# Optimization experiments

Measured on AMD Instinct MI355X. Metric: run time of the kernel, lower is better.

The kernel has to match this reference:

```python
import jax, jax.numpy as jnp
import numpy as np

S, B, D, H = 2048, 16, 1024, 1024


def setup_inputs() -> dict:
    key = jax.random.key(0)
    k1, k2, k3 = jax.random.split(key, 3)
    X = jax.random.normal(k1, (S, B, D), dtype=jnp.float32)
    hidden = jax.random.normal(k2, (B, H), dtype=jnp.float32)
    W = jax.random.normal(k3, (3 * H, D), dtype=jnp.float32) * 0.02  # nn.Linear weight [out,in]
    b = jnp.zeros((3 * H,), dtype=jnp.float32)
    return {"X": X, "hidden": hidden, "W": W, "b": b}


def reference(X, hidden, W, b):
    # window=1: source = X. Linear projection -> Z, F, O chunks.
    Y = jnp.einsum('sbd,hd->sbh', X, W) + b  # [S,B,3H]
    Z, F, O = jnp.split(Y, 3, axis=2)
    Z = jnp.tanh(Z)
    F = jax.nn.sigmoid(F)

    # ForgetMult recurrence: C_t = F_t * C_{t-1} + (1 - F_t) * Z_t, C_0 = hidden
    def step(c, fz):
        f, z = fz
        c = f * c + (1.0 - f) * z
        return c, c

    _, C = jax.lax.scan(step, hidden, (F, Z))  # C: [S,B,H]
    Hout = jax.nn.sigmoid(O) * C
    return Hout, C[-1:, :, :]
```

## Files before the change

kernel.cpp:

```cpp
#include <hip/hip_runtime.h>
#include <hip/hip_bf16.h>
#include <stdint.h>

#define S_LEN 2048
#define B_SZ  16
#define D_DIM 1024
#define H_DIM 1024
#define M_TOT (S_LEN * B_SZ)
#define N_TOT (3 * H_DIM)
#define K_TOT D_DIM

#define BM 256
#define BN 256
#define BK 64
#define NT   (K_TOT / BK)
#define NTN  (N_TOT / BN)
#define NWG  ((M_TOT / BM) * NTN)

#define NCHUNK 32
#define CLEN   64
#define NCH    (B_SZ * H_DIM)

typedef __attribute__((ext_vector_type(8))) short short8;
typedef __attribute__((ext_vector_type(4))) float f32x4;

__device__ __forceinline__ void gload_lds16(const void* g, void* l) {
  __builtin_amdgcn_global_load_lds((__attribute__((address_space(1))) void*)g,
                                   (__attribute__((address_space(3))) void*)l,
                                   16, 0, 0);
}

__device__ __forceinline__ unsigned short f2bfbits(float x) {
  union { __hip_bfloat16 h; unsigned short u; } cv;
  cv.h = __float2bfloat16(x);
  return cv.u;
}

__device__ __forceinline__ float sig_fast(float y) {
  float e = __expf(y);
  return e * __builtin_amdgcn_rcpf(1.f + e);
}
__device__ __forceinline__ float tanh_fast(float y) {
  float e = __expf(2.f * y);
  return 2.f * (e * __builtin_amdgcn_rcpf(1.f + e)) - 1.f;
}

__global__ void cvt_kernel(const float* __restrict__ in,
                           unsigned short* __restrict__ out, int n4) {
  int i = blockIdx.x * 256 + threadIdx.x;
  if (i < n4) {
    float4 v = ((const float4*)in)[i];
    ushort4 o;
    o.x = f2bfbits(v.x); o.y = f2bfbits(v.y);
    o.z = f2bfbits(v.z); o.w = f2bfbits(v.w);
    ((ushort4*)out)[i] = o;
  }
}

__global__ __launch_bounds__(512, 2) void gemm_act(
    const __hip_bfloat16* __restrict__ Xb,
    const __hip_bfloat16* __restrict__ Wb,
    const float* __restrict__ bias,
    unsigned short* __restrict__ wsZ,
    unsigned short* __restrict__ wsF,
    unsigned short* __restrict__ wsO) {
  __shared__ __align__(16) char lds[131072];

  int bid = blockIdx.x;
  int swz = (bid & 7) * (NWG >> 3) + (bid >> 3);
  int tm  = swz / NTN;
  int tn  = swz - tm * NTN;
  const int m0 = tm * BM;
  const int n0 = tn * BN;

  const int tid  = threadIdx.x;
  const int lane = tid & 63;
  const int wid  = tid >> 6;
  const int wr   = wid >> 2;
  const int wc   = wid & 3;
  const int lr   = lane & 15;
  const int lg   = lane >> 4;

  const char* Ab = (const char*)(Xb + (size_t)m0 * K_TOT);
  const char* Bb = (const char*)(Wb + (size_t)n0 * K_TOT);

  f32x4 acc[8][4];
  const f32x4 vz = {0.f, 0.f, 0.f, 0.f};
  #pragma unroll
  for (int m = 0; m < 8; ++m)
    #pragma unroll
    for (int n = 0; n < 4; ++n) acc[m][n] = vz;

  #define STAGE_HALF(gb, loff, tt, h)                                         \
    {                                                                         \
      char* l = lds + (loff) + (((tt) & 1) << 15);                            \
      _Pragma("unroll")                                                       \
      for (int j = 0; j < 2; ++j) {                                           \
        int r = (h) * 128 + j * 64 + (tid >> 3);                              \
        gload_lds16((gb) + (size_t)r * (K_TOT * 2) + (size_t)(tt) * (BK * 2)  \
                        + (((tid & 7) ^ (r & 7)) << 4),                       \
                    l + r * 128 + ((tid & 7) << 4));                          \
      }                                                                       \
    }

  #define BAR()                                                               \
    { asm volatile("" ::: "memory");                                          \
      __builtin_amdgcn_s_barrier();                                           \
      asm volatile("" ::: "memory"); }

  #define LGKM0()                                                             \
    { asm volatile("s_waitcnt lgkmcnt(0)" ::: "memory");                      \
      __builtin_amdgcn_sched_barrier(0); }

  #define VMC(n)                                                              \
    { asm volatile("s_waitcnt vmcnt(" #n ")" ::: "memory");                   \
      __builtin_amdgcn_sched_barrier(0); }

  #define READ_A(dst, tb, mh)                                                 \
    _Pragma("unroll")                                                         \
    for (int mm = 0; mm < 4; ++mm)                                            \
      _Pragma("unroll")                                                       \
      for (int ks = 0; ks < 2; ++ks) {                                        \
        int row = wr * 128 + (mh) * 64 + mm * 16 + lr;                        \
        dst[mm][ks] = *(const short8*)(lds + ((tb) << 15) + row * 128 +       \
                                       ((((ks << 2) | lg) ^ (row & 7)) << 4));\
      }

  #define READ_B(dst, tb, nh)                                                 \
    _Pragma("unroll")                                                         \
    for (int nn = 0; nn < 2; ++nn)                                            \
      _Pragma("unroll")                                                       \
      for (int ks = 0; ks < 2; ++ks) {                                        \
        int row = wc * 64 + (nh) * 32 + nn * 16 + lr;                         \
        dst[nn][ks] = *(const short8*)(lds + 65536 + ((tb) << 15) +           \
                                       row * 128 +                            \
                                       ((((ks << 2) | lg) ^ (row & 7)) << 4));\
      }

  #define MFMA_Q(mh, nh, A, Bf)                                               \
    __builtin_amdgcn_s_setprio(1);                                            \
    _Pragma("unroll")                                                         \
    for (int ks = 0; ks < 2; ++ks)                                            \
      _Pragma("unroll")                                                       \
      for (int mm = 0; mm < 4; ++mm)                                          \
        _Pragma("unroll")                                                     \
        for (int nn = 0; nn < 2; ++nn)                                        \
          acc[(mh) * 4 + mm][(nh) * 2 + nn] =                                 \
              __builtin_amdgcn_mfma_f32_16x16x32_bf16(                        \
                  A[mm][ks], Bf[nn][ks], acc[(mh) * 4 + mm][(nh) * 2 + nn],   \
                  0, 0, 0);                                                   \
    __builtin_amdgcn_s_setprio(0);

  STAGE_HALF(Ab, 0, 0, 0);
  STAGE_HALF(Ab, 0, 0, 1);
  STAGE_HALF(Bb, 65536, 0, 0);
  STAGE_HALF(Bb, 65536, 0, 1);
  STAGE_HALF(Bb, 65536, 1, 0);
  STAGE_HALF(Bb, 65536, 1, 1);
  VMC(4);
  BAR();

  short8 afr[4][2], bfr0[2][2], bfr1[2][2];
  READ_B(bfr0, 0, 0);

  for (int t = 0; t < NT; ++t) {
    const int tb = t & 1;
    READ_A(afr, tb, 0);
    if (t + 1 < NT) STAGE_HALF(Ab, 0, t + 1, 0);
    BAR();
    LGKM0();
    MFMA_Q(0, 0, afr, bfr0);
    BAR();
    READ_B(bfr1, tb, 1);
    if (t + 1 < NT) STAGE_HALF(Ab, 0, t + 1, 1);
    BAR();
    LGKM0();
    MFMA_Q(0, 1, afr, bfr1);
    BAR();
    READ_A(afr, tb, 1);
    if (t + 2 < NT) STAGE_HALF(Bb, 65536, t + 2, 0);
    BAR();
    LGKM0();
    MFMA_Q(1, 1, afr, bfr1);
    BAR();
    if (t + 2 < NT) STAGE_HALF(Bb, 65536, t + 2, 1);
    if (t < NT - 2) { VMC(4); } else { VMC(0); }
    BAR();
    MFMA_Q(1, 0, afr, bfr0);
    if (t + 1 < NT) READ_B(bfr0, tb ^ 1, 0);
    BAR();
  }

  const int chunk = n0 >> 10;
  const int hbase = (n0 & (H_DIM - 1)) + wc * 64;
  unsigned short* dst = (chunk == 0) ? wsZ : (chunk == 1) ? wsF : wsO;

  char* ep = lds + wid * 16384;
  float bv[4];
  #pragma unroll
  for (int n = 0; n < 4; ++n) bv[n] = bias[n0 + wc * 64 + n * 16 + lr];

  #pragma unroll
  for (int m = 0; m < 8; ++m)
    #pragma unroll
    for (int n = 0; n < 4; ++n)
      #pragma unroll
      for (int r = 0; r < 4; ++r) {
        int rowl = m * 16 + lg * 4 + r;
        *(unsigned short*)(ep + rowl * 128 + ((n * 16 + lr) << 1)) =
            f2bfbits(acc[m][n][r] + bv[n]);
      }

  #pragma unroll
  for (int it = 0; it < 16; ++it) {
    int rl = it * 8 + (lane >> 3);
    short8 v = *(const short8*)(ep + rl * 128 + ((lane & 7) << 4));
    size_t grow = (size_t)(m0 + wr * 128 + rl);
    *(short8*)((char*)dst + (grow * H_DIM + hbase) * 2 + ((lane & 7) << 4)) = v;
  }
}

__global__ void scan_pass1(const __hip_bfloat16* __restrict__ F,
                           const __hip_bfloat16* __restrict__ Z,
                           float* __restrict__ chP, float* __restrict__ chA) {
  int t  = blockIdx.x * 256 + threadIdx.x;
  int ch = t & (NCH - 1);
  int c  = t >> 14;
  size_t base = (size_t)c * CLEN * NCH + ch;
  float P = 1.f, A = 0.f;
  #pragma unroll 8
  for (int i = 0; i < CLEN; ++i) {
    float f = sig_fast(__bfloat162float(F[base + (size_t)i * NCH]));
    float z = tanh_fast(__bfloat162float(Z[base + (size_t)i * NCH]));
    A = fmaf(f, A, (1.f - f) * z);
    P *= f;
  }
  chP[t] = P;
  chA[t] = A;
}

__global__ void scan_mid(const float* __restrict__ chP, const float* __restrict__ chA,
                         const float* __restrict__ hidden,
                         float* __restrict__ Cst, float* __restrict__ outLast) {
  int ch = blockIdx.x * 256 + threadIdx.x;
  float c0 = hidden[ch];
  #pragma unroll
  for (int c = 0; c < NCHUNK; ++c) {
    Cst[c * NCH + ch] = c0;
    c0 = fmaf(chP[c * NCH + ch], c0, chA[c * NCH + ch]);
  }
  outLast[ch] = c0;
}

__global__ void scan_pass2(const __hip_bfloat16* __restrict__ F,
                           const __hip_bfloat16* __restrict__ Z,
                           const __hip_bfloat16* __restrict__ O,
                           const float* __restrict__ Cst,
                           float* __restrict__ out) {
  int t  = blockIdx.x * 256 + threadIdx.x;
  int ch = t & (NCH - 1);
  int c  = t >> 14;
  float C = Cst[c * NCH + ch];
  size_t base = (size_t)c * CLEN * NCH + ch;
  #pragma unroll 8
  for (int i = 0; i < CLEN; ++i) {
    size_t idx = base + (size_t)i * NCH;
    float f = sig_fast(__bfloat162float(F[idx]));
    float z = tanh_fast(__bfloat162float(Z[idx]));
    C = fmaf(f, C, (1.f - f) * z);
    out[idx] = sig_fast(__bfloat162float(O[idx])) * C;
  }
}

extern "C" void kernel_launch(void* const* d_in, const int* in_sizes, int n_in,
                              void* d_out, int out_size, void* d_ws, size_t ws_size,
                              hipStream_t stream) {
  const float* X      = (const float*)d_in[0];
  const float* hidden = (const float*)d_in[1];
  const float* W      = (const float*)d_in[2];
  const float* bias   = (const float*)d_in[3];
  float* out = (float*)d_out;

  char* ws = (char*)d_ws;
  __hip_bfloat16* Xb  = (__hip_bfloat16*)(ws);
  __hip_bfloat16* Wb  = (__hip_bfloat16*)(ws + 67108864);
  unsigned short* wsZ = (unsigned short*)(ws + 73400320);
  unsigned short* wsF = (unsigned short*)(ws + 140509184);
  unsigned short* wsO = (unsigned short*)(ws + 207618048);
  float* chP = (float*)(ws + 274726912);
  float* chA = (float*)(ws + 276824064);
  float* Cst = (float*)(ws + 278921216);

  cvt_kernel<<<(M_TOT * K_TOT / 4 + 255) / 256, 256, 0, stream>>>(X, (unsigned short*)Xb, M_TOT * K_TOT / 4);
  cvt_kernel<<<(N_TOT * K_TOT / 4 + 255) / 256, 256, 0, stream>>>(W, (unsigned short*)Wb, N_TOT * K_TOT / 4);

  gemm_act<<<NWG, 512, 0, stream>>>(Xb, Wb, bias, wsZ, wsF, wsO);

  scan_pass1<<<(NCHUNK * NCH) / 256, 256, 0, stream>>>(
      (const __hip_bfloat16*)wsF, (const __hip_bfloat16*)wsZ, chP, chA);
  scan_mid<<<NCH / 256, 256, 0, stream>>>(chP, chA, hidden, Cst, out + (size_t)M_TOT * H_DIM);
  scan_pass2<<<(NCHUNK * NCH) / 256, 256, 0, stream>>>(
      (const __hip_bfloat16*)wsF, (const __hip_bfloat16*)wsZ,
      (const __hip_bfloat16*)wsO, Cst, out);
}
```

Before: 344.0 us.

## Reorder GEMM LDS staging to match consumption order and drop barriers

Splits the staging macro into separate A and B loaders whose row assignments line up with the quarter-tiles each MFMA phase reads. Each global-to-LDS load is now issued in the phase right before its data is needed, and fine-grained vmcnt waits replace half of the per-iteration barriers, going from eight to four per K step. The goal is less barrier stalling and more overlap of loads with MFMA work. The risk is that the tighter vmcnt accounting can introduce LDS read/write hazards if any count is off.

```diff
diff --git a/kernel.cpp b/kernel.cpp
--- a/kernel.cpp
+++ b/kernel.cpp
@@ -91,14 +91,27 @@
     #pragma unroll
     for (int n = 0; n < 4; ++n) acc[m][n] = vz;
 
-  #define STAGE_HALF(gb, loff, tt, h)                                         \
+  #define STAGE_A(tt, h)                                                      \
     {                                                                         \
-      char* l = lds + (loff) + (((tt) & 1) << 15);                            \
+      char* l = lds + (((tt) & 1) << 15);                                     \
       _Pragma("unroll")                                                       \
       for (int j = 0; j < 2; ++j) {                                           \
-        int r = (h) * 128 + j * 64 + (tid >> 3);                              \
-        gload_lds16((gb) + (size_t)r * (K_TOT * 2) + (size_t)(tt) * (BK * 2)  \
-                        + (((tid & 7) ^ (r & 7)) << 4),                       \
+        int r = j * 128 + (h) * 64 + (tid >> 3);                              \
+        gload_lds16(Ab + (size_t)r * (K_TOT * 2) + (size_t)(tt) * (BK * 2)    \
+                       + (((tid & 7) ^ (r & 7)) << 4),                        \
+                    l + r * 128 + ((tid & 7) << 4));                          \
+      }                                                                       \
+    }
+
+  #define STAGE_B(tt, h)                                                      \
+    {                                                                         \
+      char* l = lds + 65536 + (((tt) & 1) << 15);                             \
+      int u = tid >> 3;                                                       \
+      _Pragma("unroll")                                                       \
+      for (int j = 0; j < 2; ++j) {                                           \
+        int r = j * 128 + (h) * 32 + (u & 31) + (u >> 5) * 64;                \
+        gload_lds16(Bb + (size_t)r * (K_TOT * 2) + (size_t)(tt) * (BK * 2)    \
+                       + (((tid & 7) ^ (r & 7)) << 4),                        \
                     l + r * 128 + ((tid & 7) << 4));                          \
       }                                                                       \
     }
@@ -151,13 +164,12 @@
                   0, 0, 0);                                                   \
     __builtin_amdgcn_s_setprio(0);
 
-  STAGE_HALF(Ab, 0, 0, 0);
-  STAGE_HALF(Ab, 0, 0, 1);
-  STAGE_HALF(Bb, 65536, 0, 0);
-  STAGE_HALF(Bb, 65536, 0, 1);
-  STAGE_HALF(Bb, 65536, 1, 0);
-  STAGE_HALF(Bb, 65536, 1, 1);
-  VMC(4);
+  STAGE_A(0, 0);
+  STAGE_B(0, 0);
+  STAGE_B(0, 1);
+  STAGE_A(0, 1);
+  STAGE_B(1, 0);
+  VMC(6);
   BAR();
 
   short8 afr[4][2], bfr0[2][2], bfr1[2][2];
@@ -166,35 +178,34 @@
   for (int t = 0; t < NT; ++t) {
     const int tb = t & 1;
     READ_A(afr, tb, 0);
-    if (t + 1 < NT) STAGE_HALF(Ab, 0, t + 1, 0);
+    if (t + 1 < NT) { STAGE_A(t + 1, 0); VMC(6); } else { VMC(2); }
     BAR();
     LGKM0();
     MFMA_Q(0, 0, afr, bfr0);
-    BAR();
     READ_B(bfr1, tb, 1);
-    if (t + 1 < NT) STAGE_HALF(Ab, 0, t + 1, 1);
+    if (t + 1 < NT) { STAGE_B(t + 1, 1); VMC(6); } else { VMC(0); }
     BAR();
     LGKM0();
     MFMA_Q(0, 1, afr, bfr1);
-    BAR();
     READ_A(afr, tb, 1);
-    if (t + 2 < NT) STAGE_HALF(Bb, 65536, t + 2, 0);
+    if (t + 1 < NT) { STAGE_A(t + 1, 1); VMC(6); } else { VMC(0); }
     BAR();
     LGKM0();
     MFMA_Q(1, 1, afr, bfr1);
+    if (t + 2 < NT)      { STAGE_B(t + 2, 0); VMC(6); }
+    else if (t + 1 < NT) { VMC(4); }
+    else                 { VMC(0); }
     BAR();
-    if (t + 2 < NT) STAGE_HALF(Bb, 65536, t + 2, 1);
-    if (t < NT - 2) { VMC(4); } else { VMC(0); }
-    BAR();
+    LGKM0();
     MFMA_Q(1, 0, afr, bfr0);
     if (t + 1 < NT) READ_B(bfr0, tb ^ 1, 0);
-    BAR();
   }
 
   const int chunk = n0 >> 10;
   const int hbase = (n0 & (H_DIM - 1)) + wc * 64;
   unsigned short* dst = (chunk == 0) ? wsZ : (chunk == 1) ? wsF : wsO;
 
+  BAR();
   char* ep = lds + wid * 16384;
   float bv[4];
   #pragma unroll
```

Result: faster. 336.9 us (-2.1%).

## Use 4-wave 256x256 GEMM tiles with per-wave 128x128 output and fewer barriers

Applied to the files above, without the earlier changes.

The GEMM block drops from 8 waves to 4, so each wave computes a 128x128 sub-tile (64 accumulator fragments) instead of 128x64, raising register-level reuse of A and B fragments. The staging schedule is reworked so each thread issues more global-to-LDS loads per phase, with explicit vmcnt waits, and several intra-iteration barriers are removed. The epilogue is resized for the wider per-wave tile. This cuts LDS reads per MFMA and barrier overhead, but doubles accumulator register pressure, halves occupancy, and risks spills or less latency hiding.

```diff
diff --git a/kernel.cpp b/kernel.cpp
--- a/kernel.cpp
+++ b/kernel.cpp
@@ -57,7 +57,7 @@
   }
 }
 
-__global__ __launch_bounds__(512, 2) void gemm_act(
+__global__ __launch_bounds__(256, 1) void gemm_act(
     const __hip_bfloat16* __restrict__ Xb,
     const __hip_bfloat16* __restrict__ Wb,
     const float* __restrict__ bias,
@@ -76,27 +76,28 @@
   const int tid  = threadIdx.x;
   const int lane = tid & 63;
   const int wid  = tid >> 6;
-  const int wr   = wid >> 2;
-  const int wc   = wid & 3;
+  const int wr   = wid >> 1;
+  const int wc   = wid & 1;
   const int lr   = lane & 15;
   const int lg   = lane >> 4;
 
   const char* Ab = (const char*)(Xb + (size_t)m0 * K_TOT);
   const char* Bb = (const char*)(Wb + (size_t)n0 * K_TOT);
 
-  f32x4 acc[8][4];
+  f32x4 acc[8][8];
   const f32x4 vz = {0.f, 0.f, 0.f, 0.f};
   #pragma unroll
   for (int m = 0; m < 8; ++m)
     #pragma unroll
-    for (int n = 0; n < 4; ++n) acc[m][n] = vz;
-
-  #define STAGE_HALF(gb, loff, tt, h)                                         \
+    for (int n = 0; n < 8; ++n) acc[m][n] = vz;
+
+  #define STAGE(gb, loff, tt, h)                                              \
     {                                                                         \
       char* l = lds + (loff) + (((tt) & 1) << 15);                            \
+      int u = tid >> 3;                                                       \
       _Pragma("unroll")                                                       \
-      for (int j = 0; j < 2; ++j) {                                           \
-        int r = (h) * 128 + j * 64 + (tid >> 3);                              \
+      for (int j = 0; j < 4; ++j) {                                           \
+        int r = ((j & 1) << 7) + (h) * 64 + ((j >> 1) << 5) + u;              \
         gload_lds16((gb) + (size_t)r * (K_TOT * 2) + (size_t)(tt) * (BK * 2)  \
                         + (((tid & 7) ^ (r & 7)) << 4),                       \
                     l + r * 128 + ((tid & 7) << 4));                          \
@@ -128,10 +129,10 @@
 
   #define READ_B(dst, tb, nh)                                                 \
     _Pragma("unroll")                                                         \
-    for (int nn = 0; nn < 2; ++nn)                                            \
+    for (int nn = 0; nn < 4; ++nn)                                            \
       _Pragma("unroll")                                                       \
       for (int ks = 0; ks < 2; ++ks) {                                        \
-        int row = wc * 64 + (nh) * 32 + nn * 16 + lr;                         \
+        int row = wc * 128 + (nh) * 64 + nn * 16 + lr;                        \
         dst[nn][ks] = *(const short8*)(lds + 65536 + ((tb) << 15) +           \
                                        row * 128 +                            \
                                        ((((ks << 2) | lg) ^ (row & 7)) << 4));\
@@ -144,79 +145,77 @@
       _Pragma("unroll")                                                       \
       for (int mm = 0; mm < 4; ++mm)                                          \
         _Pragma("unroll")                                                     \
-        for (int nn = 0; nn < 2; ++nn)                                        \
-          acc[(mh) * 4 + mm][(nh) * 2 + nn] =                                 \
+        for (int nn = 0; nn < 4; ++nn)                                        \
+          acc[(mh) * 4 + mm][(nh) * 4 + nn] =                                 \
               __builtin_amdgcn_mfma_f32_16x16x32_bf16(                        \
-                  A[mm][ks], Bf[nn][ks], acc[(mh) * 4 + mm][(nh) * 2 + nn],   \
+                  A[mm][ks], Bf[nn][ks], acc[(mh) * 4 + mm][(nh) * 4 + nn],   \
                   0, 0, 0);                                                   \
     __builtin_amdgcn_s_setprio(0);
 
-  STAGE_HALF(Ab, 0, 0, 0);
-  STAGE_HALF(Ab, 0, 0, 1);
-  STAGE_HALF(Bb, 65536, 0, 0);
-  STAGE_HALF(Bb, 65536, 0, 1);
-  STAGE_HALF(Bb, 65536, 1, 0);
-  STAGE_HALF(Bb, 65536, 1, 1);
-  VMC(4);
+  STAGE(Ab, 0, 0, 0);
+  STAGE(Bb, 65536, 0, 0);
+  STAGE(Bb, 65536, 0, 1);
+  STAGE(Ab, 0, 0, 1);
+  STAGE(Bb, 65536, 1, 0);
+  VMC(12);
   BAR();
 
-  short8 afr[4][2], bfr0[2][2], bfr1[2][2];
+  short8 afr[4][2], bfr0[4][2], bfr1[4][2];
   READ_B(bfr0, 0, 0);
 
   for (int t = 0; t < NT; ++t) {
     const int tb = t & 1;
     READ_A(afr, tb, 0);
-    if (t + 1 < NT) STAGE_HALF(Ab, 0, t + 1, 0);
+    if (t + 1 < NT) { STAGE(Ab, 0, t + 1, 0); VMC(12); } else { VMC(4); }
     BAR();
     LGKM0();
     MFMA_Q(0, 0, afr, bfr0);
-    BAR();
     READ_B(bfr1, tb, 1);
-    if (t + 1 < NT) STAGE_HALF(Ab, 0, t + 1, 1);
+    if (t + 1 < NT) { STAGE(Bb, 65536, t + 1, 1); VMC(12); } else { VMC(0); }
     BAR();
     LGKM0();
     MFMA_Q(0, 1, afr, bfr1);
-    BAR();
     READ_A(afr, tb, 1);
-    if (t + 2 < NT) STAGE_HALF(Bb, 65536, t + 2, 0);
+    if (t + 1 < NT) { STAGE(Ab, 0, t + 1, 1); VMC(12); } else { VMC(0); }
     BAR();
     LGKM0();
     MFMA_Q(1, 1, afr, bfr1);
+    if (t + 2 < NT)      { STAGE(Bb, 65536, t + 2, 0); VMC(12); }
+    else if (t + 1 < NT) { VMC(8); }
+    else                 { VMC(0); }
     BAR();
-    if (t + 2 < NT) STAGE_HALF(Bb, 65536, t + 2, 1);
-    if (t < NT - 2) { VMC(4); } else { VMC(0); }
-    BAR();
+    LGKM0();
     MFMA_Q(1, 0, afr, bfr0);
     if (t + 1 < NT) READ_B(bfr0, tb ^ 1, 0);
-    BAR();
   }
 
   const int chunk = n0 >> 10;
-  const int hbase = (n0 & (H_DIM - 1)) + wc * 64;
+  const int hbase = (n0 & (H_DIM - 1)) + wc * 128;
   unsigned short* dst = (chunk == 0) ? wsZ : (chunk == 1) ? wsF : wsO;
 
-  char* ep = lds + wid * 16384;
-  float bv[4];
-  #pragma unroll
-  for (int n = 0; n < 4; ++n) bv[n] = bias[n0 + wc * 64 + n * 16 + lr];
+  BAR();
+  char* ep = lds + wid * 32768;
+  float bv[8];
+  #pragma unroll
+  for (int n = 0; n < 8; ++n) bv[n] = bias[n0 + wc * 128 + n * 16 + lr];
 
   #pragma unroll
   for (int m = 0; m < 8; ++m)
     #pragma unroll
-    for (int n = 0; n < 4; ++n)
+    for (int n = 0; n < 8; ++n)
       #pragma unroll
       for (int r = 0; r < 4; ++r) {
         int rowl = m * 16 + lg * 4 + r;
-        *(unsigned short*)(ep + rowl * 128 + ((n * 16 + lr) << 1)) =
+        *(unsigned short*)(ep + rowl * 256 + ((n * 16 + lr) << 1)) =
             f2bfbits(acc[m][n][r] + bv[n]);
       }
 
   #pragma unroll
-  for (int it = 0; it < 16; ++it) {
-    int rl = it * 8 + (lane >> 3);
-    short8 v = *(const short8*)(ep + rl * 128 + ((lane & 7) << 4));
+  for (int it = 0; it < 32; ++it) {
+    int rl = it * 4 + (lane >> 4);
+    short8 v = *(const short8*)(ep + rl * 256 + ((lane & 15) << 4));
     size_t grow = (size_t)(m0 + wr * 128 + rl);
-    *(short8*)((char*)dst + (grow * H_DIM + hbase) * 2 + ((lane & 7) << 4)) = v;
+    *(short8*)((char*)dst + (grow * H_DIM + hbase) * 2 + ((lane & 15) << 4)) = v;
   }
 }
 
@@ -294,11 +293,12 @@
   cvt_kernel<<<(M_TOT * K_TOT / 4 + 255) / 256, 256, 0, stream>>>(X, (unsigned short*)Xb, M_TOT * K_TOT / 4);
   cvt_kernel<<<(N_TOT * K_TOT / 4 + 255) / 256, 256, 0, stream>>>(W, (unsigned short*)Wb, N_TOT * K_TOT / 4);
 
-  gemm_act<<<NWG, 512, 0, stream>>>(Xb, Wb, bias, wsZ, wsF, wsO);
+  gemm_act<<<NWG, 256, 0, stream>>>(Xb, Wb, bias, wsZ, wsF, wsO);
 
   scan_pass1<<<(NCHUNK * NCH) / 256, 256, 0, stream>>>(
       (const __hip_bfloat16*)wsF, (const __hip_bfloat16*)wsZ, chP, chA);
-  scan_mid<<<NCH / 256, 256, 0, stream>>>(chP, chA, hidden, Cst, out + (size_t)M_TOT * H_DIM);
+  scan_mid<<<NCH / 256, 256, 0, stream>>>(chP, chA, hidden, Cst,
+                                          out + (size_t)M_TOT * H_DIM);
   scan_pass2<<<(NCHUNK * NCH) / 256, 256, 0, stream>>>(
       (const __hip_bfloat16*)wsF, (const __hip_bfloat16*)wsZ,
       (const __hip_bfloat16*)wsO, Cst, out);
```

After: 350.6 us. About the same (+1.9%).
